# Performance work log

Measured on AMD Instinct MI355X. Metric: run time of the kernel, lower is better.

Reference implementation:

```python
import jax, jax.numpy as jnp
import numpy as np

G = 8            # grid_size
G2 = G * G       # total_grid_size = 64
NS = 2.0         # neighborhood_size
H = 64           # h_dim
A = 1024         # bottleneck_dim == attention_dim
S = 32           # number of sequences
N = 64           # pedestrians per sequence
P = 4096         # scene boundary points per sequence (down_samples)
B = S * N        # total batch = 2048


def setup_inputs() -> dict:
    key = jax.random.key(0)
    ks = jax.random.split(key, 16)
    starts = jnp.arange(S, dtype=jnp.int32) * N
    seq_start_end = jnp.stack([starts, starts + N], axis=1)  # (S, 2) uniform groups
    return {
        "h_states": jax.random.normal(ks[0], (1, B, H), jnp.float32),
        "end_pos": jax.random.normal(ks[1], (B, 2), jnp.float32),
        "rel_pos": jax.random.normal(ks[2], (B, 2), jnp.float32) * 0.1,
        "scene_info": jax.random.normal(ks[3], (S, P, 2), jnp.float32),
        # Attention_Decoder params (soft attention over G2 grid cells, encoder_dim=1)
        "W_enc": jax.random.normal(ks[4], (1, A), jnp.float32) * 0.05,
        "b_enc": jnp.zeros((A,), jnp.float32),
        "W_dec": jax.random.normal(ks[5], (H, A), jnp.float32) * 0.05,
        "b_dec": jnp.zeros((A,), jnp.float32),
        "w_full": jax.random.normal(ks[6], (A, 1), jnp.float32) * 0.05,
        "b_full": jnp.zeros((1,), jnp.float32),
        "W_out": jax.random.normal(ks[7], (1 + H + 4, A), jnp.float32) * 0.05,  # [ctx, h, embed_info]
        "b_out": jnp.zeros((A,), jnp.float32),
        # mlp_pool: Linear(A, A) + BatchNorm1d + ReLU
        "W_mlp": jax.random.normal(ks[8], (A, A), jnp.float32) * 0.05,
        "b_mlp": jnp.zeros((A,), jnp.float32),
        "gamma": jnp.ones((A,), jnp.float32),
        "beta": jnp.zeros((A,), jnp.float32),
        "seq_start_end": seq_start_end,
    }


def _occupancy(end_pos, scene_info, num_seqs, peds, grid_size, ns):
    """Vectorized per-pedestrian grid-cell binning + scatter-add occupancy.
    end_pos: (num_seqs*peds, 2), scene_info: (num_seqs, P, 2) -> (B, G2)."""
    g2 = grid_size * grid_size
    b = num_seqs * peds
    ep = end_pos.reshape(num_seqs, peds, 1, 2)
    sx = scene_info[:, None, :, 0]  # (S, 1, P)
    sy = scene_info[:, None, :, 1]
    tl_x = ep[..., 0] - ns / 2
    tl_y = ep[..., 1] + ns / 2
    br_x = ep[..., 0] + ns / 2
    br_y = ep[..., 1] - ns / 2
    cell_x = jnp.floor((sx - tl_x) / ns * grid_size)   # (S, N, P)
    cell_y = jnp.floor((tl_y - sy) / ns * grid_size)
    cell = (cell_x + cell_y * grid_size).astype(jnp.int32)
    # point is out-of-bound if outside the ped's neighborhood box (matches torch mask)
    oob = (sx >= br_x) | (sx <= tl_x) | (sy >= tl_y) | (sy <= br_y)
    ped = jnp.arange(b, dtype=jnp.int32).reshape(num_seqs, peds, 1)
    # torch scatters masked points into slot 0 then drops it; we use one dump slot at the end
    idx = jnp.where(oob, b * g2, ped * g2 + cell)      # (S, N, P)
    counts = jax.ops.segment_sum(
        jnp.ones(idx.size, jnp.float32), idx.reshape(-1), num_segments=b * g2 + 1)
    return counts[:-1].reshape(b, g2)


def reference(h_states, end_pos, rel_pos, scene_info,
              W_enc, b_enc, W_dec, b_dec, w_full, b_full,
              W_out, b_out, W_mlp, b_mlp, gamma, beta, seq_start_end):
    num_seqs = seq_start_end.shape[0]
    b = end_pos.shape[0]
    peds = b // num_seqs
    occ = _occupancy(end_pos, scene_info, num_seqs, peds, G, NS)   # (B, G2)
    enc = occ[..., None]                                           # (B, G2, 1)
    h = h_states.reshape(b, -1)                                    # (B, H)
    embed_info = jnp.concatenate([end_pos, rel_pos], axis=1)       # (B, 4)
    # soft attention over the G2 grid cells conditioned on the decoder hidden state
    att = jax.nn.relu(enc @ W_enc + b_enc + (h @ W_dec + b_dec)[:, None, :])  # (B, G2, A)
    e = (att @ w_full)[..., 0] + b_full                            # (B, G2)
    alpha = jax.nn.softmax(e, axis=1)
    ctx = jnp.sum(alpha[..., None] * enc, axis=1)                  # (B, 1)
    pool = jnp.concatenate([ctx, h, embed_info], axis=1) @ W_out + b_out  # (B, A)
    # mlp_pool: Linear -> BatchNorm1d (training stats, biased var) -> ReLU
    y = pool @ W_mlp + b_mlp
    mu = jnp.mean(y, axis=0)
    var = jnp.mean((y - mu) ** 2, axis=0)
    y = gamma * (y - mu) * jax.lax.rsqrt(var + 1e-5) + beta
    return jax.nn.relu(y)
```

## Files before the change

kernel.cpp:

```cpp
#include <hip/hip_runtime.h>
#include <hip/hip_bf16.h>


#define NPED 2048
#define NA   1024
#define NG2  64
#define NPTS 4096

typedef unsigned short ushort_t;
typedef __attribute__((ext_vector_type(8))) short bf16x8;
typedef __attribute__((ext_vector_type(4))) float f32x4;

struct PrepPtrs { const void* p[16]; };

__device__ __forceinline__ float bf2f(ushort_t u) {
  return __uint_as_float(((unsigned int)u) << 16);
}
__device__ __forceinline__ ushort_t f2bf(float f) {
  __hip_bfloat16 b = __float2bfloat16(f);
  return *reinterpret_cast<ushort_t*>(&b);
}
__device__ __forceinline__ int block_flag(const ushort_t* h) {
  __shared__ int bad_sh;
  if (threadIdx.x == 0) bad_sh = 0;
  __syncthreads();
  float v = bf2f(h[threadIdx.x & 255]);
  if (!(fabsf(v) <= 1e4f)) atomicOr(&bad_sh, 1);
  __syncthreads();
  return (bad_sh == 0) ? 1 : 0;
}
__device__ __forceinline__ float lde(const void* p, size_t i, int fl) {
  return fl ? bf2f(((const ushort_t*)p)[i]) : ((const float*)p)[i];
}

__device__ __forceinline__ void tp_body(const void* in, int fl, int job,
                                        int Kin, int Kpad, ushort_t* out) {
  __shared__ ushort_t t[32][40];
  int n0 = (job & 31) * 32, k0 = (job >> 5) * 32;
  int r = threadIdx.x >> 3, c4 = (threadIdx.x & 7) * 4;
  ushort4 v = make_ushort4(0, 0, 0, 0);
  if (k0 + r < Kin) {
    size_t off = (size_t)(k0 + r) * 1024 + n0 + c4;
    if (fl) {
      v = *(const ushort4*)((const ushort_t*)in + off);
    } else {
      float4 f = *(const float4*)((const float*)in + off);
      v = make_ushort4(f2bf(f.x), f2bf(f.y), f2bf(f.z), f2bf(f.w));
    }
  }
  *(ushort4*)(&t[r][c4]) = v;
  __syncthreads();
  int n = threadIdx.x >> 3, kk = (threadIdx.x & 7) * 4;
  ushort4 o = make_ushort4(t[kk][n], t[kk + 1][n], t[kk + 2][n], t[kk + 3][n]);
  *(ushort4*)(out + (size_t)(n0 + n) * Kpad + k0 + kk) = o;
}

__global__ __launch_bounds__(256) void k_prep(PrepPtrs ptrs,
                                              float* __restrict__ conv,
                                              ushort_t* __restrict__ hbf,
                                              ushort_t* __restrict__ WdecT,
                                              ushort_t* __restrict__ WoutT,
                                              ushort_t* __restrict__ WmlpT,
                                              ushort_t* __restrict__ Xcat0,
                                              float* __restrict__ occ,
                                              float* __restrict__ stats) {
  int b = blockIdx.x;
  int fl = block_flag((const ushort_t*)ptrs.p[0]);
  if (b < 273) {
    const int ends[12] = {4096, 8192, 270336, 271360, 272384, 273408,
                          274432, 275456, 276480, 277504, 278528, 279552};
    int idx = (b * 256 + threadIdx.x) * 4;
    int seg = 0, base = 0;
#pragma unroll
    for (int s = 0; s < 11; s++) {
      if (idx >= ends[s]) { seg = s + 1; base = ends[s]; }
    }
    int off = idx - base;
    float4 o;
    if (fl) {
      const unsigned int* src = (const unsigned int*)ptrs.p[4 + seg];
      uint2 u = *(const uint2*)(src + (off >> 1));
      o.x = __uint_as_float((u.x & 0xFFFFu) << 16);
      o.y = __uint_as_float(u.x & 0xFFFF0000u);
      o.z = __uint_as_float((u.y & 0xFFFFu) << 16);
      o.w = __uint_as_float(u.y & 0xFFFF0000u);
    } else {
      o = *(const float4*)((const float*)ptrs.p[4 + seg] + off);
    }
    *(float4*)(conv + idx) = o;
  } else if (b < 401) {
    int i = (b - 273) * 256 + threadIdx.x;
    if (fl) {
      ((ushort4*)hbf)[i] = ((const ushort4*)ptrs.p[0])[i];
    } else {
      float4 f = ((const float4*)ptrs.p[0])[i];
      ((ushort4*)hbf)[i] = make_ushort4(f2bf(f.x), f2bf(f.y), f2bf(f.z), f2bf(f.w));
    }
  } else if (b < 465) {
    tp_body(ptrs.p[1], fl, b - 401, 64, 64, WdecT);
  } else if (b < 561) {
    const void* wout1 = fl ? (const void*)((const ushort_t*)ptrs.p[2] + 1024)
                           : (const void*)((const float*)ptrs.p[2] + 1024);
    tp_body(wout1, fl, b - 465, 68, 96, WoutT);
  } else if (b < 1585) {
    tp_body(ptrs.p[3], fl, b - 561, 1024, 1024, WmlpT);
  } else if (b < 1777) {
    int flat = (b - 1585) * 256 + threadIdx.x;
    int e4 = flat * 4;
    int r = e4 / 96, c = e4 - r * 96;
    ushort4 v = make_ushort4(0, 0, 0, 0);
    if (c < 64) {
      if (fl) v = *(const ushort4*)((const ushort_t*)ptrs.p[0] + r * 64 + c);
      else {
        float4 f = *(const float4*)((const float*)ptrs.p[0] + r * 64 + c);
        v = make_ushort4(f2bf(f.x), f2bf(f.y), f2bf(f.z), f2bf(f.w));
      }
    } else if (c == 64) {
      v.x = f2bf(lde(ptrs.p[4], 2 * r, fl));
      v.y = f2bf(lde(ptrs.p[4], 2 * r + 1, fl));
      v.z = f2bf(lde(ptrs.p[5], 2 * r, fl));
      v.w = f2bf(lde(ptrs.p[5], 2 * r + 1, fl));
    }
    *(ushort4*)(Xcat0 + e4) = v;
  } else if (b < 3825) {
    int i = b - 1777;
    int s = i >> 6;
    __shared__ float cnt[NG2];
    if (threadIdx.x < NG2) cnt[threadIdx.x] = 0.0f;
    __syncthreads();
    float ex = lde(ptrs.p[4], 2 * i, fl), ey = lde(ptrs.p[4], 2 * i + 1, fl);
    float tlx = ex - 1.0f, tly = ey + 1.0f, brx = ex + 1.0f, bry = ey - 1.0f;
    const void* scn = ptrs.p[6];
    for (int p = threadIdx.x; p < NPTS; p += 256) {
      size_t o2 = (size_t)s * NPTS * 2 + 2 * p;
      float sx = lde(scn, o2, fl), sy = lde(scn, o2 + 1, fl);
      bool oob = (sx >= brx) || (sx <= tlx) || (sy >= tly) || (sy <= bry);
      if (!oob) {
        int cx = (int)floorf((sx - tlx) * 0.5f * 8.0f);
        int cy = (int)floorf((tly - sy) * 0.5f * 8.0f);
        int cell = cx + cy * 8;
        if (cell >= 0 && cell < NG2) atomicAdd(&cnt[cell], 1.0f);
      }
    }
    __syncthreads();
    if (threadIdx.x < NG2) occ[i * NG2 + threadIdx.x] = cnt[threadIdx.x];
  } else {
#pragma unroll
    for (int k = 0; k < 8; k++) stats[threadIdx.x + 256 * k] = 0.0f;
  }
}

template <int K, int EPI>
__device__ __forceinline__ void mgemm_body(
    ushort_t* As, ushort_t* Bs,
    const ushort_t* __restrict__ A, int lda,
    const ushort_t* __restrict__ BT, int ldb,
    const float* __restrict__ bias1, const float* __restrict__ bias2,
    ushort_t* __restrict__ outb, float* __restrict__ outf,
    float* __restrict__ stats) {
  int tid = threadIdx.x;
  int m0 = blockIdx.x * 64, n0 = blockIdx.y * 128;
  int wave = tid >> 6, lane = tid & 63, l15 = lane & 15, kg = lane >> 4;
  f32x4 acc[4][2] = {};
  int ar = tid >> 2, ag = tid & 3;
  int aswz = ag ^ ((ar >> 1) & 3);
  for (int k0 = 0; k0 < K; k0 += 32) {
    uint4 av = *(const uint4*)(A + (size_t)(m0 + ar) * lda + k0 + ag * 8);
    *(uint4*)(&As[ar * 32 + aswz * 8]) = av;
#pragma unroll
    for (int i = 0; i < 2; i++) {
      int c = tid + i * 256;
      int br = c >> 2, bg = c & 3;
      int bswz = bg ^ ((br >> 1) & 3);
      uint4 bv = *(const uint4*)(BT + (size_t)(n0 + br) * ldb + k0 + bg * 8);
      *(uint4*)(&Bs[br * 32 + bswz * 8]) = bv;
    }
    __syncthreads();
    bf16x8 af[4], bfr[2];
#pragma unroll
    for (int mt = 0; mt < 4; mt++) {
      int row = mt * 16 + l15;
      int swz = kg ^ ((row >> 1) & 3);
      af[mt] = *(const bf16x8*)(&As[row * 32 + swz * 8]);
    }
#pragma unroll
    for (int nt = 0; nt < 2; nt++) {
      int row = wave * 32 + nt * 16 + l15;
      int swz = kg ^ ((row >> 1) & 3);
      bfr[nt] = *(const bf16x8*)(&Bs[row * 32 + swz * 8]);
    }
#pragma unroll
    for (int mt = 0; mt < 4; mt++)
#pragma unroll
      for (int nt = 0; nt < 2; nt++)
        acc[mt][nt] = __builtin_amdgcn_mfma_f32_16x16x32_bf16(af[mt], bfr[nt], acc[mt][nt], 0, 0, 0);
    __syncthreads();
  }
#pragma unroll
  for (int nt = 0; nt < 2; nt++) {
    int col = n0 + wave * 32 + nt * 16 + l15;
    float bsum = (EPI == 0) ? (bias1[col] + bias2[col]) : bias1[col];
    float s1 = 0.0f, s2 = 0.0f;
#pragma unroll
    for (int mt = 0; mt < 4; mt++) {
#pragma unroll
      for (int r = 0; r < 4; r++) {
        int rowm = m0 + mt * 16 + kg * 4 + r;
        float v = acc[mt][nt][r] + bsum;
        if (EPI == 3) outf[(size_t)rowm * 1024 + col] = v;
        else outb[(size_t)rowm * 1024 + col] = f2bf(v);
        if (EPI == 2) { s1 += v; s2 = fmaf(v, v, s2); }
      }
    }
    if (EPI == 2) {
      s1 += __shfl_down(s1, 16); s2 += __shfl_down(s2, 16);
      s1 += __shfl_down(s1, 32); s2 += __shfl_down(s2, 32);
      if (lane < 16) {
        atomicAdd(&stats[col], s1);
        atomicAdd(&stats[1024 + col], s2);
      }
    }
  }
}

__global__ __launch_bounds__(256) void k_gemm2(
    const ushort_t* __restrict__ hbf, const ushort_t* __restrict__ WdecT,
    const float* __restrict__ benc, const float* __restrict__ bdec,
    ushort_t* __restrict__ hd_out,
    const ushort_t* __restrict__ Xcat0, const ushort_t* __restrict__ WoutT,
    const float* __restrict__ bout, float* __restrict__ P1) {
  __shared__ ushort_t As[64 * 32];
  __shared__ ushort_t Bs[128 * 32];
  if (blockIdx.z == 0)
    mgemm_body<64, 0>(As, Bs, hbf, 64, WdecT, 64, benc, bdec, hd_out, nullptr, nullptr);
  else
    mgemm_body<96, 3>(As, Bs, Xcat0, 96, WoutT, 96, bout, nullptr, nullptr, P1, nullptr);
}

__global__ __launch_bounds__(256) void k_mgemm_y(
    const ushort_t* __restrict__ A, const ushort_t* __restrict__ BT,
    const float* __restrict__ bias1, ushort_t* __restrict__ outb,
    float* __restrict__ stats) {
  __shared__ ushort_t As[64 * 32];
  __shared__ ushort_t Bs[128 * 32];
  mgemm_body<1024, 2>(As, Bs, A, 1024, BT, 1024, bias1, nullptr, outb, nullptr, stats);
}

__global__ __launch_bounds__(256) void k_ectx(
    const float* __restrict__ occ,
    const float* __restrict__ Wenc, const float* __restrict__ wfull,
    const float* __restrict__ w0, const float* __restrict__ P1,
    const ushort_t* __restrict__ hd, ushort_t* __restrict__ pool) {
  int wave = threadIdx.x >> 6, lane = threadIdx.x & 63;
  int p = blockIdx.x * 4 + wave;
  __shared__ float occ_sh[4][64];
  occ_sh[wave][lane] = occ[p * 64 + lane];
  float hdv[16], we[16], wf[16];
#pragma unroll
  for (int j = 0; j < 16; j++) {
    int a = lane + j * 64;
    hdv[j] = bf2f(hd[(size_t)p * 1024 + a]);
    we[j] = Wenc[a];
    wf[j] = wfull[a];
  }
  float e_mine = 0.0f;
  for (int g = 0; g < 64; g++) {
    float c = occ_sh[wave][g];
    float s = 0.0f;
#pragma unroll
    for (int j = 0; j < 16; j++)
      s += fmaxf(fmaf(c, we[j], hdv[j]), 0.0f) * wf[j];
#pragma unroll
    for (int off = 32; off > 0; off >>= 1) s += __shfl_xor(s, off);
    if (lane == g) e_mine = s;
  }
  float m = e_mine;
#pragma unroll
  for (int off = 32; off > 0; off >>= 1) m = fmaxf(m, __shfl_xor(m, off));
  float xe = __expf(e_mine - m);
  float den = xe;
#pragma unroll
  for (int off = 32; off > 0; off >>= 1) den += __shfl_xor(den, off);
  float cp = xe * occ_sh[wave][lane];
#pragma unroll
  for (int off = 32; off > 0; off >>= 1) cp += __shfl_xor(cp, off);
  float ctx = cp / den;
#pragma unroll
  for (int j = 0; j < 16; j++) {
    int a = lane + j * 64;
    pool[(size_t)p * 1024 + a] = f2bf(fmaf(ctx, w0[a], P1[(size_t)p * 1024 + a]));
  }
}

__global__ void k_norm(const ushort_t* __restrict__ y_mf,
                       const float* __restrict__ stats,
                       const float* __restrict__ gamma, const float* __restrict__ beta,
                       const ushort_t* __restrict__ hsrc, void* __restrict__ out) {
  int fl = block_flag(hsrc);
  int idx = (blockIdx.x * 256 + threadIdx.x) * 4;
  int col = idx & (NA - 1);
  float vv[4];
#pragma unroll
  for (int j = 0; j < 4; j++) vv[j] = bf2f(y_mf[idx + j]);
  float4 s1 = *(const float4*)(stats + col);
  float4 s2 = *(const float4*)(stats + NA + col);
  float4 gm = *(const float4*)(gamma + col);
  float4 bt = *(const float4*)(beta + col);
  const float ib = 1.0f / 2048.0f;
  float m1[4] = {s1.x, s1.y, s1.z, s1.w};
  float m2[4] = {s2.x, s2.y, s2.z, s2.w};
  float gg[4] = {gm.x, gm.y, gm.z, gm.w};
  float bb[4] = {bt.x, bt.y, bt.z, bt.w};
  float o[4];
#pragma unroll
  for (int j = 0; j < 4; j++) {
    float mu = m1[j] * ib;
    float var = fmaf(-mu, mu, m2[j] * ib);
    o[j] = fmaxf(fmaf(gg[j] * (vv[j] - mu), rsqrtf(var + 1e-5f), bb[j]), 0.0f);
  }
  if (fl) {
    ushort4 ov = make_ushort4(f2bf(o[0]), f2bf(o[1]), f2bf(o[2]), f2bf(o[3]));
    *(ushort4*)((ushort_t*)out + idx) = ov;
  } else {
    *(float4*)((float*)out + idx) = make_float4(o[0], o[1], o[2], o[3]);
  }
}

extern "C" void kernel_launch(void* const* d_in, const int* in_sizes, int n_in,
                              void* d_out, int out_size, void* d_ws, size_t ws_size,
                              hipStream_t stream) {
  float* ws = (float*)d_ws;
  float* conv   = ws;
  float* c_Wenc = conv + 270336;
  float* c_benc = conv + 271360;
  float* c_bdec = conv + 272384;
  float* c_wful = conv + 273408;
  float* c_bout = conv + 274432;
  float* c_bmlp = conv + 275456;
  float* c_gam  = conv + 276480;
  float* c_bet  = conv + 277504;
  float* c_w0   = conv + 278528;
  float* occ    = ws + 280576;
  float* stats  = ws + 411648;
  float* P1     = ws + 413696;
  ushort_t* u0    = (ushort_t*)(ws + 2510848);
  ushort_t* hbf   = u0;
  ushort_t* WdecT = u0 + 131072;
  ushort_t* WoutT = u0 + 196608;
  ushort_t* WmlpT = u0 + 294912;
  ushort_t* Xcat0 = u0 + 1343488;
  ushort_t* y_mf  = u0 + 1540096;
  ushort_t* hd_bf   = (ushort_t*)d_out;
  ushort_t* pool_mf = (ushort_t*)d_out;

  PrepPtrs ptrs;
  ptrs.p[0] = d_in[0];
  ptrs.p[1] = d_in[6];
  ptrs.p[2] = d_in[10];
  ptrs.p[3] = d_in[12];
  ptrs.p[4] = d_in[1];
  ptrs.p[5] = d_in[2];
  ptrs.p[6] = d_in[3];
  ptrs.p[7] = d_in[4];
  ptrs.p[8] = d_in[5];
  ptrs.p[9] = d_in[7];
  ptrs.p[10] = d_in[8];
  ptrs.p[11] = d_in[11];
  ptrs.p[12] = d_in[13];
  ptrs.p[13] = d_in[14];
  ptrs.p[14] = d_in[15];
  ptrs.p[15] = d_in[10];

  k_prep<<<3826, 256, 0, stream>>>(ptrs, conv, hbf, WdecT, WoutT, WmlpT,
                                   Xcat0, occ, stats);

  k_gemm2<<<dim3(32, 8, 2), 256, 0, stream>>>(hbf, WdecT, c_benc, c_bdec, hd_bf,
                                              Xcat0, WoutT, c_bout, P1);

  k_ectx<<<512, 256, 0, stream>>>(occ, c_Wenc, c_wful, c_w0, P1, hd_bf, pool_mf);

  k_mgemm_y<<<dim3(32, 8), 256, 0, stream>>>(pool_mf, WmlpT, c_bmlp, y_mf, stats);

  k_norm<<<2048, 256, 0, stream>>>(y_mf, stats, c_gam, c_bet,
                                   (const ushort_t*)d_in[0], d_out);
}
```

Baseline: 163.6 us.

## Fuse all stages into one persistent kernel with software grid barriers

Replaces five kernel launches with one persistent 512-block kernel. The stages (prep, the two small GEMMs, attention/context, the y GEMM, and the norm) are separated by atomic-counter grid barriers. The y GEMM tile is also changed from 64x128 to 64x64 so all 512 blocks have work. This is meant to remove launch gaps and inter-kernel drain, at the cost of spin-wait barriers, a reliance on all blocks being co-resident, and an extra memset launch.

```diff
diff --git a/kernel.cpp b/kernel.cpp
--- a/kernel.cpp
+++ b/kernel.cpp
@@ -2,10 +2,9 @@
 #include <hip/hip_bf16.h>
 
 
-#define NPED 2048
-#define NA   1024
 #define NG2  64
 #define NPTS 4096
+#define NBLK 512
 
 typedef unsigned short ushort_t;
 typedef __attribute__((ext_vector_type(8))) short bf16x8;
@@ -20,17 +19,19 @@
   __hip_bfloat16 b = __float2bfloat16(f);
   return *reinterpret_cast<ushort_t*>(&b);
 }
-__device__ __forceinline__ int block_flag(const ushort_t* h) {
-  __shared__ int bad_sh;
-  if (threadIdx.x == 0) bad_sh = 0;
-  __syncthreads();
-  float v = bf2f(h[threadIdx.x & 255]);
-  if (!(fabsf(v) <= 1e4f)) atomicOr(&bad_sh, 1);
-  __syncthreads();
-  return (bad_sh == 0) ? 1 : 0;
-}
 __device__ __forceinline__ float lde(const void* p, size_t i, int fl) {
   return fl ? bf2f(((const ushort_t*)p)[i]) : ((const float*)p)[i];
+}
+
+__device__ __forceinline__ void gbar(unsigned* cnt, unsigned want) {
+  __syncthreads();
+  if (threadIdx.x == 0) {
+    __threadfence();
+    atomicAdd(cnt, 1u);
+    while (atomicAdd(cnt, 0u) < want) __builtin_amdgcn_s_sleep(2);
+    __threadfence();
+  }
+  __syncthreads();
 }
 
 __device__ __forceinline__ void tp_body(const void* in, int fl, int job,
@@ -55,17 +56,10 @@
   *(ushort4*)(out + (size_t)(n0 + n) * Kpad + k0 + kk) = o;
 }
 
-__global__ __launch_bounds__(256) void k_prep(PrepPtrs ptrs,
-                                              float* __restrict__ conv,
-                                              ushort_t* __restrict__ hbf,
-                                              ushort_t* __restrict__ WdecT,
-                                              ushort_t* __restrict__ WoutT,
-                                              ushort_t* __restrict__ WmlpT,
-                                              ushort_t* __restrict__ Xcat0,
-                                              float* __restrict__ occ,
-                                              float* __restrict__ stats) {
-  int b = blockIdx.x;
-  int fl = block_flag((const ushort_t*)ptrs.p[0]);
+__device__ void prep_job(const PrepPtrs& ptrs, int fl, int b,
+                         float* conv, ushort_t* hbf, ushort_t* WdecT,
+                         ushort_t* WoutT, ushort_t* WmlpT, ushort_t* Xcat0,
+                         float* occ, float* stats) {
   if (b < 273) {
     const int ends[12] = {4096, 8192, 270336, 271360, 272384, 273408,
                           274432, 275456, 276480, 277504, 278528, 279552};
@@ -125,8 +119,8 @@
   } else if (b < 3825) {
     int i = b - 1777;
     int s = i >> 6;
-    __shared__ float cnt[NG2];
-    if (threadIdx.x < NG2) cnt[threadIdx.x] = 0.0f;
+    __shared__ float cnth[NG2];
+    if (threadIdx.x < NG2) cnth[threadIdx.x] = 0.0f;
     __syncthreads();
     float ex = lde(ptrs.p[4], 2 * i, fl), ey = lde(ptrs.p[4], 2 * i + 1, fl);
     float tlx = ex - 1.0f, tly = ey + 1.0f, brx = ex + 1.0f, bry = ey - 1.0f;
@@ -139,11 +133,11 @@
         int cx = (int)floorf((sx - tlx) * 0.5f * 8.0f);
         int cy = (int)floorf((tly - sy) * 0.5f * 8.0f);
         int cell = cx + cy * 8;
-        if (cell >= 0 && cell < NG2) atomicAdd(&cnt[cell], 1.0f);
+        if (cell >= 0 && cell < NG2) atomicAdd(&cnth[cell], 1.0f);
       }
     }
     __syncthreads();
-    if (threadIdx.x < NG2) occ[i * NG2 + threadIdx.x] = cnt[threadIdx.x];
+    if (threadIdx.x < NG2) occ[i * NG2 + threadIdx.x] = cnth[threadIdx.x];
   } else {
 #pragma unroll
     for (int k = 0; k < 8; k++) stats[threadIdx.x + 256 * k] = 0.0f;
@@ -151,15 +145,12 @@
 }
 
 template <int K, int EPI>
-__device__ __forceinline__ void mgemm_body(
-    ushort_t* As, ushort_t* Bs,
-    const ushort_t* __restrict__ A, int lda,
-    const ushort_t* __restrict__ BT, int ldb,
-    const float* __restrict__ bias1, const float* __restrict__ bias2,
-    ushort_t* __restrict__ outb, float* __restrict__ outf,
-    float* __restrict__ stats) {
+__device__ void mgemm_body(ushort_t* As, ushort_t* Bs, int m0, int n0,
+                           const ushort_t* __restrict__ A, int lda,
+                           const ushort_t* __restrict__ BT, int ldb,
+                           const float* __restrict__ bias1, const float* __restrict__ bias2,
+                           ushort_t* __restrict__ outb, float* __restrict__ outf) {
   int tid = threadIdx.x;
-  int m0 = blockIdx.x * 64, n0 = blockIdx.y * 128;
   int wave = tid >> 6, lane = tid & 63, l15 = lane & 15, kg = lane >> 4;
   f32x4 acc[4][2] = {};
   int ar = tid >> 2, ag = tid & 3;
@@ -200,7 +191,6 @@
   for (int nt = 0; nt < 2; nt++) {
     int col = n0 + wave * 32 + nt * 16 + l15;
     float bsum = (EPI == 0) ? (bias1[col] + bias2[col]) : bias1[col];
-    float s1 = 0.0f, s2 = 0.0f;
 #pragma unroll
     for (int mt = 0; mt < 4; mt++) {
 #pragma unroll
@@ -209,50 +199,74 @@
         float v = acc[mt][nt][r] + bsum;
         if (EPI == 3) outf[(size_t)rowm * 1024 + col] = v;
         else outb[(size_t)rowm * 1024 + col] = f2bf(v);
-        if (EPI == 2) { s1 += v; s2 = fmaf(v, v, s2); }
       }
     }
-    if (EPI == 2) {
-      s1 += __shfl_down(s1, 16); s2 += __shfl_down(s2, 16);
-      s1 += __shfl_down(s1, 32); s2 += __shfl_down(s2, 32);
-      if (lane < 16) {
-        atomicAdd(&stats[col], s1);
-        atomicAdd(&stats[1024 + col], s2);
-      }
-    }
-  }
-}
-
-__global__ __launch_bounds__(256) void k_gemm2(
-    const ushort_t* __restrict__ hbf, const ushort_t* __restrict__ WdecT,
-    const float* __restrict__ benc, const float* __restrict__ bdec,
-    ushort_t* __restrict__ hd_out,
-    const ushort_t* __restrict__ Xcat0, const ushort_t* __restrict__ WoutT,
-    const float* __restrict__ bout, float* __restrict__ P1) {
-  __shared__ ushort_t As[64 * 32];
-  __shared__ ushort_t Bs[128 * 32];
-  if (blockIdx.z == 0)
-    mgemm_body<64, 0>(As, Bs, hbf, 64, WdecT, 64, benc, bdec, hd_out, nullptr, nullptr);
-  else
-    mgemm_body<96, 3>(As, Bs, Xcat0, 96, WoutT, 96, bout, nullptr, nullptr, P1, nullptr);
-}
-
-__global__ __launch_bounds__(256) void k_mgemm_y(
-    const ushort_t* __restrict__ A, const ushort_t* __restrict__ BT,
-    const float* __restrict__ bias1, ushort_t* __restrict__ outb,
-    float* __restrict__ stats) {
-  __shared__ ushort_t As[64 * 32];
-  __shared__ ushort_t Bs[128 * 32];
-  mgemm_body<1024, 2>(As, Bs, A, 1024, BT, 1024, bias1, nullptr, outb, nullptr, stats);
-}
-
-__global__ __launch_bounds__(256) void k_ectx(
-    const float* __restrict__ occ,
-    const float* __restrict__ Wenc, const float* __restrict__ wfull,
-    const float* __restrict__ w0, const float* __restrict__ P1,
-    const ushort_t* __restrict__ hd, ushort_t* __restrict__ pool) {
+  }
+}
+
+__device__ void ygemm_job(ushort_t* As, ushort_t* Bs, int m0, int n0,
+                          const ushort_t* __restrict__ A,
+                          const ushort_t* __restrict__ BT,
+                          const float* __restrict__ bias1,
+                          ushort_t* __restrict__ outb, float* __restrict__ stats) {
+  int tid = threadIdx.x;
+  int wave = tid >> 6, lane = tid & 63, l15 = lane & 15, kg = lane >> 4;
+  f32x4 acc[4] = {};
+  int ar = tid >> 2, ag = tid & 3;
+  int aswz = ag ^ ((ar >> 1) & 3);
+  for (int k0 = 0; k0 < 1024; k0 += 32) {
+    uint4 av = *(const uint4*)(A + (size_t)(m0 + ar) * 1024 + k0 + ag * 8);
+    *(uint4*)(&As[ar * 32 + aswz * 8]) = av;
+    {
+      int br = tid >> 2, bg = tid & 3;
+      int bswz = bg ^ ((br >> 1) & 3);
+      uint4 bv = *(const uint4*)(BT + (size_t)(n0 + br) * 1024 + k0 + bg * 8);
+      *(uint4*)(&Bs[br * 32 + bswz * 8]) = bv;
+    }
+    __syncthreads();
+    bf16x8 af[4], bfr;
+#pragma unroll
+    for (int mt = 0; mt < 4; mt++) {
+      int row = mt * 16 + l15;
+      int swz = kg ^ ((row >> 1) & 3);
+      af[mt] = *(const bf16x8*)(&As[row * 32 + swz * 8]);
+    }
+    {
+      int row = wave * 16 + l15;
+      int swz = kg ^ ((row >> 1) & 3);
+      bfr = *(const bf16x8*)(&Bs[row * 32 + swz * 8]);
+    }
+#pragma unroll
+    for (int mt = 0; mt < 4; mt++)
+      acc[mt] = __builtin_amdgcn_mfma_f32_16x16x32_bf16(af[mt], bfr, acc[mt], 0, 0, 0);
+    __syncthreads();
+  }
+  int col = n0 + wave * 16 + l15;
+  float bsum = bias1[col];
+  float s1 = 0.0f, s2 = 0.0f;
+#pragma unroll
+  for (int mt = 0; mt < 4; mt++) {
+#pragma unroll
+    for (int r = 0; r < 4; r++) {
+      int rowm = m0 + mt * 16 + kg * 4 + r;
+      float v = acc[mt][r] + bsum;
+      outb[(size_t)rowm * 1024 + col] = f2bf(v);
+      s1 += v; s2 = fmaf(v, v, s2);
+    }
+  }
+  s1 += __shfl_down(s1, 16); s2 += __shfl_down(s2, 16);
+  s1 += __shfl_down(s1, 32); s2 += __shfl_down(s2, 32);
+  if (lane < 16) {
+    atomicAdd(&stats[col], s1);
+    atomicAdd(&stats[1024 + col], s2);
+  }
+}
+
+__device__ void ectx_job(int pbase, const float* occ, const float* Wenc,
+                         const float* wfull, const float* w0, const float* P1,
+                         const ushort_t* hd, ushort_t* pool) {
   int wave = threadIdx.x >> 6, lane = threadIdx.x & 63;
-  int p = blockIdx.x * 4 + wave;
+  int p = pbase + wave;
   __shared__ float occ_sh[4][64];
   occ_sh[wave][lane] = occ[p * 64 + lane];
   float hdv[16], we[16], wf[16];
@@ -292,18 +306,15 @@
   }
 }
 
-__global__ void k_norm(const ushort_t* __restrict__ y_mf,
-                       const float* __restrict__ stats,
-                       const float* __restrict__ gamma, const float* __restrict__ beta,
-                       const ushort_t* __restrict__ hsrc, void* __restrict__ out) {
-  int fl = block_flag(hsrc);
-  int idx = (blockIdx.x * 256 + threadIdx.x) * 4;
-  int col = idx & (NA - 1);
+__device__ void norm_job(int j, int fl, const ushort_t* y_mf, const float* stats,
+                         const float* gamma, const float* beta, void* out) {
+  int idx = (j * 256 + threadIdx.x) * 4;
+  int col = idx & 1023;
   float vv[4];
 #pragma unroll
-  for (int j = 0; j < 4; j++) vv[j] = bf2f(y_mf[idx + j]);
+  for (int q = 0; q < 4; q++) vv[q] = bf2f(y_mf[idx + q]);
   float4 s1 = *(const float4*)(stats + col);
-  float4 s2 = *(const float4*)(stats + NA + col);
+  float4 s2 = *(const float4*)(stats + 1024 + col);
   float4 gm = *(const float4*)(gamma + col);
   float4 bt = *(const float4*)(beta + col);
   const float ib = 1.0f / 2048.0f;
@@ -313,10 +324,10 @@
   float bb[4] = {bt.x, bt.y, bt.z, bt.w};
   float o[4];
 #pragma unroll
-  for (int j = 0; j < 4; j++) {
-    float mu = m1[j] * ib;
-    float var = fmaf(-mu, mu, m2[j] * ib);
-    o[j] = fmaxf(fmaf(gg[j] * (vv[j] - mu), rsqrtf(var + 1e-5f), bb[j]), 0.0f);
+  for (int q = 0; q < 4; q++) {
+    float mu = m1[q] * ib;
+    float var = fmaf(-mu, mu, m2[q] * ib);
+    o[q] = fmaxf(fmaf(gg[q] * (vv[q] - mu), rsqrtf(var + 1e-5f), bb[q]), 0.0f);
   }
   if (fl) {
     ushort4 ov = make_ushort4(f2bf(o[0]), f2bf(o[1]), f2bf(o[2]), f2bf(o[3]));
@@ -326,10 +337,9 @@
   }
 }
 
-extern "C" void kernel_launch(void* const* d_in, const int* in_sizes, int n_in,
-                              void* d_out, int out_size, void* d_ws, size_t ws_size,
-                              hipStream_t stream) {
-  float* ws = (float*)d_ws;
+__global__ __launch_bounds__(256, 2) void k_mega(
+    PrepPtrs ptrs, float* __restrict__ ws, unsigned* __restrict__ cnt,
+    ushort_t* __restrict__ dout) {
   float* conv   = ws;
   float* c_Wenc = conv + 270336;
   float* c_benc = conv + 271360;
@@ -350,8 +360,55 @@
   ushort_t* WmlpT = u0 + 294912;
   ushort_t* Xcat0 = u0 + 1343488;
   ushort_t* y_mf  = u0 + 1540096;
-  ushort_t* hd_bf   = (ushort_t*)d_out;
-  ushort_t* pool_mf = (ushort_t*)d_out;
+
+  __shared__ ushort_t As[64 * 32];
+  __shared__ ushort_t Bs[128 * 32];
+
+  __shared__ int bad_sh;
+  if (threadIdx.x == 0) bad_sh = 0;
+  __syncthreads();
+  {
+    float v = bf2f(((const ushort_t*)ptrs.p[0])[threadIdx.x]);
+    if (!(fabsf(v) <= 1e4f)) atomicOr(&bad_sh, 1);
+  }
+  __syncthreads();
+  int fl = (bad_sh == 0) ? 1 : 0;
+
+  int bid = blockIdx.x;
+
+  for (int j = bid; j < 3826; j += NBLK) {
+    prep_job(ptrs, fl, j, conv, hbf, WdecT, WoutT, WmlpT, Xcat0, occ, stats);
+    __syncthreads();
+  }
+  gbar(cnt, NBLK);
+
+  {
+    int m0 = (bid & 31) * 64, n0 = ((bid >> 5) & 7) * 128;
+    if ((bid >> 8) == 0)
+      mgemm_body<64, 0>(As, Bs, m0, n0, hbf, 64, WdecT, 64, c_benc, c_bdec,
+                        dout, nullptr);
+    else
+      mgemm_body<96, 3>(As, Bs, m0, n0, Xcat0, 96, WoutT, 96, c_bout, nullptr,
+                        nullptr, P1);
+  }
+  gbar(cnt, 2 * NBLK);
+
+  ectx_job(bid * 4, occ, c_Wenc, c_wful, c_w0, P1, dout, dout);
+  gbar(cnt, 3 * NBLK);
+
+  ygemm_job(As, Bs, (bid & 31) * 64, (bid >> 5) * 64, dout, WmlpT, c_bmlp,
+            y_mf, stats);
+  gbar(cnt, 4 * NBLK);
+
+  for (int j = bid; j < 2048; j += NBLK)
+    norm_job(j, fl, y_mf, stats, c_gam, c_bet, dout);
+}
+
+extern "C" void kernel_launch(void* const* d_in, const int* in_sizes, int n_in,
+                              void* d_out, int out_size, void* d_ws, size_t ws_size,
+                              hipStream_t stream) {
+  float* ws = (float*)d_ws;
+  unsigned* cnt = (unsigned*)((char*)d_ws + 17317888);
 
   PrepPtrs ptrs;
   ptrs.p[0] = d_in[0];
@@ -371,16 +428,7 @@
   ptrs.p[14] = d_in[15];
   ptrs.p[15] = d_in[10];
 
-  k_prep<<<3826, 256, 0, stream>>>(ptrs, conv, hbf, WdecT, WoutT, WmlpT,
-                                   Xcat0, occ, stats);
-
-  k_gemm2<<<dim3(32, 8, 2), 256, 0, stream>>>(hbf, WdecT, c_benc, c_bdec, hd_bf,
-                                              Xcat0, WoutT, c_bout, P1);
-
-  k_ectx<<<512, 256, 0, stream>>>(occ, c_Wenc, c_wful, c_w0, P1, hd_bf, pool_mf);
-
-  k_mgemm_y<<<dim3(32, 8), 256, 0, stream>>>(pool_mf, WmlpT, c_bmlp, y_mf, stats);
-
-  k_norm<<<2048, 256, 0, stream>>>(y_mf, stats, c_gam, c_bet,
-                                   (const ushort_t*)d_in[0], d_out);
-}
+  hipMemsetAsync(cnt, 0, sizeof(unsigned), stream);
+
+  k_mega<<<NBLK, 256, 0, stream>>>(ptrs, ws, cnt, (ushort_t*)d_out);
+}
```

Measured after the change: 365.8 us. 2.24x slower.

## Drop dead scene/position conversion and retile MLP GEMM to 64x64 blocks

Applied to the files above, without the earlier changes.

The prep kernel no longer converts end_pos, rel_pos and scene_info into the fp32 workspace. Those copies were unused, because the occupancy and Xcat paths already read the original inputs. This removes about 270K floats of read and write traffic and 264 blocks, and the workspace offsets are repacked to match. The 1024x1024 MLP GEMM gets its own kernel with 64x64 tiles and one 16-column slice per wave, launched as 512 blocks instead of 256, to fill more compute units. The cost is less B-tile reuse per block and twice as many stats atomics.

```diff
diff --git a/kernel.cpp b/kernel.cpp
--- a/kernel.cpp
+++ b/kernel.cpp
@@ -2,8 +2,6 @@
 #include <hip/hip_bf16.h>
 
 
-#define NPED 2048
-#define NA   1024
 #define NG2  64
 #define NPTS 4096
 
@@ -19,6 +17,9 @@
 __device__ __forceinline__ ushort_t f2bf(float f) {
   __hip_bfloat16 b = __float2bfloat16(f);
   return *reinterpret_cast<ushort_t*>(&b);
+}
+__device__ __forceinline__ float lde(const void* p, size_t i, int fl) {
+  return fl ? bf2f(((const ushort_t*)p)[i]) : ((const float*)p)[i];
 }
 __device__ __forceinline__ int block_flag(const ushort_t* h) {
   __shared__ int bad_sh;
@@ -28,9 +29,6 @@
   if (!(fabsf(v) <= 1e4f)) atomicOr(&bad_sh, 1);
   __syncthreads();
   return (bad_sh == 0) ? 1 : 0;
-}
-__device__ __forceinline__ float lde(const void* p, size_t i, int fl) {
-  return fl ? bf2f(((const ushort_t*)p)[i]) : ((const float*)p)[i];
 }
 
 __device__ __forceinline__ void tp_body(const void* in, int fl, int job,
@@ -66,46 +64,39 @@
                                               float* __restrict__ stats) {
   int b = blockIdx.x;
   int fl = block_flag((const ushort_t*)ptrs.p[0]);
-  if (b < 273) {
-    const int ends[12] = {4096, 8192, 270336, 271360, 272384, 273408,
-                          274432, 275456, 276480, 277504, 278528, 279552};
+  if (b < 9) {
     int idx = (b * 256 + threadIdx.x) * 4;
-    int seg = 0, base = 0;
-#pragma unroll
-    for (int s = 0; s < 11; s++) {
-      if (idx >= ends[s]) { seg = s + 1; base = ends[s]; }
-    }
-    int off = idx - base;
+    int seg = idx >> 10, off = idx & 1023;
     float4 o;
     if (fl) {
-      const unsigned int* src = (const unsigned int*)ptrs.p[4 + seg];
+      const unsigned int* src = (const unsigned int*)ptrs.p[7 + seg];
       uint2 u = *(const uint2*)(src + (off >> 1));
       o.x = __uint_as_float((u.x & 0xFFFFu) << 16);
       o.y = __uint_as_float(u.x & 0xFFFF0000u);
       o.z = __uint_as_float((u.y & 0xFFFFu) << 16);
       o.w = __uint_as_float(u.y & 0xFFFF0000u);
     } else {
-      o = *(const float4*)((const float*)ptrs.p[4 + seg] + off);
+      o = *(const float4*)((const float*)ptrs.p[7 + seg] + off);
     }
     *(float4*)(conv + idx) = o;
-  } else if (b < 401) {
-    int i = (b - 273) * 256 + threadIdx.x;
+  } else if (b < 137) {
+    int i = (b - 9) * 256 + threadIdx.x;
     if (fl) {
       ((ushort4*)hbf)[i] = ((const ushort4*)ptrs.p[0])[i];
     } else {
       float4 f = ((const float4*)ptrs.p[0])[i];
       ((ushort4*)hbf)[i] = make_ushort4(f2bf(f.x), f2bf(f.y), f2bf(f.z), f2bf(f.w));
     }
-  } else if (b < 465) {
-    tp_body(ptrs.p[1], fl, b - 401, 64, 64, WdecT);
-  } else if (b < 561) {
+  } else if (b < 201) {
+    tp_body(ptrs.p[1], fl, b - 137, 64, 64, WdecT);
+  } else if (b < 297) {
     const void* wout1 = fl ? (const void*)((const ushort_t*)ptrs.p[2] + 1024)
                            : (const void*)((const float*)ptrs.p[2] + 1024);
-    tp_body(wout1, fl, b - 465, 68, 96, WoutT);
-  } else if (b < 1585) {
-    tp_body(ptrs.p[3], fl, b - 561, 1024, 1024, WmlpT);
-  } else if (b < 1777) {
-    int flat = (b - 1585) * 256 + threadIdx.x;
+    tp_body(wout1, fl, b - 201, 68, 96, WoutT);
+  } else if (b < 1321) {
+    tp_body(ptrs.p[3], fl, b - 297, 1024, 1024, WmlpT);
+  } else if (b < 1513) {
+    int flat = (b - 1321) * 256 + threadIdx.x;
     int e4 = flat * 4;
     int r = e4 / 96, c = e4 - r * 96;
     ushort4 v = make_ushort4(0, 0, 0, 0);
@@ -122,11 +113,11 @@
       v.w = f2bf(lde(ptrs.p[5], 2 * r + 1, fl));
     }
     *(ushort4*)(Xcat0 + e4) = v;
-  } else if (b < 3825) {
-    int i = b - 1777;
+  } else if (b < 3561) {
+    int i = b - 1513;
     int s = i >> 6;
-    __shared__ float cnt[NG2];
-    if (threadIdx.x < NG2) cnt[threadIdx.x] = 0.0f;
+    __shared__ float cnth[NG2];
+    if (threadIdx.x < NG2) cnth[threadIdx.x] = 0.0f;
     __syncthreads();
     float ex = lde(ptrs.p[4], 2 * i, fl), ey = lde(ptrs.p[4], 2 * i + 1, fl);
     float tlx = ex - 1.0f, tly = ey + 1.0f, brx = ex + 1.0f, bry = ey - 1.0f;
@@ -139,11 +130,11 @@
         int cx = (int)floorf((sx - tlx) * 0.5f * 8.0f);
         int cy = (int)floorf((tly - sy) * 0.5f * 8.0f);
         int cell = cx + cy * 8;
-        if (cell >= 0 && cell < NG2) atomicAdd(&cnt[cell], 1.0f);
+        if (cell >= 0 && cell < NG2) atomicAdd(&cnth[cell], 1.0f);
       }
     }
     __syncthreads();
-    if (threadIdx.x < NG2) occ[i * NG2 + threadIdx.x] = cnt[threadIdx.x];
+    if (threadIdx.x < NG2) occ[i * NG2 + threadIdx.x] = cnth[threadIdx.x];
   } else {
 #pragma unroll
     for (int k = 0; k < 8; k++) stats[threadIdx.x + 256 * k] = 0.0f;
@@ -152,14 +143,12 @@
 
 template <int K, int EPI>
 __device__ __forceinline__ void mgemm_body(
-    ushort_t* As, ushort_t* Bs,
+    ushort_t* As, ushort_t* Bs, int m0, int n0,
     const ushort_t* __restrict__ A, int lda,
     const ushort_t* __restrict__ BT, int ldb,
     const float* __restrict__ bias1, const float* __restrict__ bias2,
-    ushort_t* __restrict__ outb, float* __restrict__ outf,
-    float* __restrict__ stats) {
+    ushort_t* __restrict__ outb, float* __restrict__ outf) {
   int tid = threadIdx.x;
-  int m0 = blockIdx.x * 64, n0 = blockIdx.y * 128;
   int wave = tid >> 6, lane = tid & 63, l15 = lane & 15, kg = lane >> 4;
   f32x4 acc[4][2] = {};
   int ar = tid >> 2, ag = tid & 3;
@@ -200,7 +189,6 @@
   for (int nt = 0; nt < 2; nt++) {
     int col = n0 + wave * 32 + nt * 16 + l15;
     float bsum = (EPI == 0) ? (bias1[col] + bias2[col]) : bias1[col];
-    float s1 = 0.0f, s2 = 0.0f;
 #pragma unroll
     for (int mt = 0; mt < 4; mt++) {
 #pragma unroll
@@ -209,15 +197,6 @@
         float v = acc[mt][nt][r] + bsum;
         if (EPI == 3) outf[(size_t)rowm * 1024 + col] = v;
         else outb[(size_t)rowm * 1024 + col] = f2bf(v);
-        if (EPI == 2) { s1 += v; s2 = fmaf(v, v, s2); }
-      }
-    }
-    if (EPI == 2) {
-      s1 += __shfl_down(s1, 16); s2 += __shfl_down(s2, 16);
-      s1 += __shfl_down(s1, 32); s2 += __shfl_down(s2, 32);
-      if (lane < 16) {
-        atomicAdd(&stats[col], s1);
-        atomicAdd(&stats[1024 + col], s2);
       }
     }
   }
@@ -231,19 +210,71 @@
     const float* __restrict__ bout, float* __restrict__ P1) {
   __shared__ ushort_t As[64 * 32];
   __shared__ ushort_t Bs[128 * 32];
+  int m0 = blockIdx.x * 64, n0 = blockIdx.y * 128;
   if (blockIdx.z == 0)
-    mgemm_body<64, 0>(As, Bs, hbf, 64, WdecT, 64, benc, bdec, hd_out, nullptr, nullptr);
+    mgemm_body<64, 0>(As, Bs, m0, n0, hbf, 64, WdecT, 64, benc, bdec, hd_out, nullptr);
   else
-    mgemm_body<96, 3>(As, Bs, Xcat0, 96, WoutT, 96, bout, nullptr, nullptr, P1, nullptr);
-}
-
-__global__ __launch_bounds__(256) void k_mgemm_y(
+    mgemm_body<96, 3>(As, Bs, m0, n0, Xcat0, 96, WoutT, 96, bout, nullptr, nullptr, P1);
+}
+
+__global__ __launch_bounds__(256) void k_ygemm(
     const ushort_t* __restrict__ A, const ushort_t* __restrict__ BT,
     const float* __restrict__ bias1, ushort_t* __restrict__ outb,
     float* __restrict__ stats) {
   __shared__ ushort_t As[64 * 32];
-  __shared__ ushort_t Bs[128 * 32];
-  mgemm_body<1024, 2>(As, Bs, A, 1024, BT, 1024, bias1, nullptr, outb, nullptr, stats);
+  __shared__ ushort_t Bs[64 * 32];
+  int m0 = blockIdx.x * 64, n0 = blockIdx.y * 64;
+  int tid = threadIdx.x;
+  int wave = tid >> 6, lane = tid & 63, l15 = lane & 15, kg = lane >> 4;
+  f32x4 acc[4] = {};
+  int ar = tid >> 2, ag = tid & 3;
+  int aswz = ag ^ ((ar >> 1) & 3);
+  for (int k0 = 0; k0 < 1024; k0 += 32) {
+    uint4 av = *(const uint4*)(A + (size_t)(m0 + ar) * 1024 + k0 + ag * 8);
+    *(uint4*)(&As[ar * 32 + aswz * 8]) = av;
+    {
+      int br = tid >> 2, bg = tid & 3;
+      int bswz = bg ^ ((br >> 1) & 3);
+      uint4 bv = *(const uint4*)(BT + (size_t)(n0 + br) * 1024 + k0 + bg * 8);
+      *(uint4*)(&Bs[br * 32 + bswz * 8]) = bv;
+    }
+    __syncthreads();
+    bf16x8 af[4], bfr;
+#pragma unroll
+    for (int mt = 0; mt < 4; mt++) {
+      int row = mt * 16 + l15;
+      int swz = kg ^ ((row >> 1) & 3);
+      af[mt] = *(const bf16x8*)(&As[row * 32 + swz * 8]);
+    }
+    {
+      int row = wave * 16 + l15;
+      int swz = kg ^ ((row >> 1) & 3);
+      bfr = *(const bf16x8*)(&Bs[row * 32 + swz * 8]);
+    }
+#pragma unroll
+    for (int mt = 0; mt < 4; mt++)
+      acc[mt] = __builtin_amdgcn_mfma_f32_16x16x32_bf16(af[mt], bfr, acc[mt], 0, 0, 0);
+    __syncthreads();
+  }
+  int col = n0 + wave * 16 + l15;
+  float bsum = bias1[col];
+  float s1 = 0.0f, s2 = 0.0f;
+#pragma unroll
+  for (int mt = 0; mt < 4; mt++) {
+#pragma unroll
+    for (int r = 0; r < 4; r++) {
+      int rowm = m0 + mt * 16 + kg * 4 + r;
+      float v = acc[mt][r] + bsum;
+      outb[(size_t)rowm * 1024 + col] = f2bf(v);
+      s1 += v; s2 = fmaf(v, v, s2);
+    }
+  }
+  s1 += __shfl_down(s1, 16); s2 += __shfl_down(s2, 16);
+  s1 += __shfl_down(s1, 32); s2 += __shfl_down(s2, 32);
+  if (lane < 16) {
+    atomicAdd(&stats[col], s1);
+    atomicAdd(&stats[1024 + col], s2);
+  }
 }
 
 __global__ __launch_bounds__(256) void k_ectx(
@@ -298,12 +329,12 @@
                        const ushort_t* __restrict__ hsrc, void* __restrict__ out) {
   int fl = block_flag(hsrc);
   int idx = (blockIdx.x * 256 + threadIdx.x) * 4;
-  int col = idx & (NA - 1);
+  int col = idx & 1023;
   float vv[4];
 #pragma unroll
   for (int j = 0; j < 4; j++) vv[j] = bf2f(y_mf[idx + j]);
   float4 s1 = *(const float4*)(stats + col);
-  float4 s2 = *(const float4*)(stats + NA + col);
+  float4 s2 = *(const float4*)(stats + 1024 + col);
   float4 gm = *(const float4*)(gamma + col);
   float4 bt = *(const float4*)(beta + col);
   const float ib = 1.0f / 2048.0f;
@@ -331,19 +362,19 @@
                               hipStream_t stream) {
   float* ws = (float*)d_ws;
   float* conv   = ws;
-  float* c_Wenc = conv + 270336;
-  float* c_benc = conv + 271360;
-  float* c_bdec = conv + 272384;
-  float* c_wful = conv + 273408;
-  float* c_bout = conv + 274432;
-  float* c_bmlp = conv + 275456;
-  float* c_gam  = conv + 276480;
-  float* c_bet  = conv + 277504;
-  float* c_w0   = conv + 278528;
-  float* occ    = ws + 280576;
-  float* stats  = ws + 411648;
-  float* P1     = ws + 413696;
-  ushort_t* u0    = (ushort_t*)(ws + 2510848);
+  float* c_Wenc = conv + 0;
+  float* c_benc = conv + 1024;
+  float* c_bdec = conv + 2048;
+  float* c_wful = conv + 3072;
+  float* c_bout = conv + 4096;
+  float* c_bmlp = conv + 5120;
+  float* c_gam  = conv + 6144;
+  float* c_bet  = conv + 7168;
+  float* c_w0   = conv + 8192;
+  float* occ    = ws + 9216;
+  float* stats  = ws + 140288;
+  float* P1     = ws + 142336;
+  ushort_t* u0    = (ushort_t*)(ws + 2239488);
   ushort_t* hbf   = u0;
   ushort_t* WdecT = u0 + 131072;
   ushort_t* WoutT = u0 + 196608;
@@ -361,9 +392,9 @@
   ptrs.p[4] = d_in[1];
   ptrs.p[5] = d_in[2];
   ptrs.p[6] = d_in[3];
-  ptrs.p[7] = d_in[4];
-  ptrs.p[8] = d_in[5];
-  ptrs.p[9] = d_in[7];
+  ptrs.p[7]  = d_in[4];
+  ptrs.p[8]  = d_in[5];
+  ptrs.p[9]  = d_in[7];
   ptrs.p[10] = d_in[8];
   ptrs.p[11] = d_in[11];
   ptrs.p[12] = d_in[13];
@@ -371,7 +402,7 @@
   ptrs.p[14] = d_in[15];
   ptrs.p[15] = d_in[10];
 
-  k_prep<<<3826, 256, 0, stream>>>(ptrs, conv, hbf, WdecT, WoutT, WmlpT,
+  k_prep<<<3562, 256, 0, stream>>>(ptrs, conv, hbf, WdecT, WoutT, WmlpT,
                                    Xcat0, occ, stats);
 
   k_gemm2<<<dim3(32, 8, 2), 256, 0, stream>>>(hbf, WdecT, c_benc, c_bdec, hd_bf,
@@ -379,7 +410,7 @@
 
   k_ectx<<<512, 256, 0, stream>>>(occ, c_Wenc, c_wful, c_w0, P1, hd_bf, pool_mf);
 
-  k_mgemm_y<<<dim3(32, 8), 256, 0, stream>>>(pool_mf, WmlpT, c_bmlp, y_mf, stats);
+  k_ygemm<<<dim3(32, 16), 256, 0, stream>>>(pool_mf, WmlpT, c_bmlp, y_mf, stats);
 
   k_norm<<<2048, 256, 0, stream>>>(y_mf, stats, c_gam, c_bet,
                                    (const ushort_t*)d_in[0], d_out);
```

Result: no change. 162.6 us (-0.6%).
